# Kernel optimization log

Hardware: AMD Instinct MI355X
Metric: run time of the kernel (lower is better)

The kernel has to match this reference:

```python
import jax, jax.numpy as jnp
import numpy as np

B, S, H = 4, 2048, 1024

def setup_inputs() -> dict:
    key = jax.random.key(0)
    ks = jax.random.split(key, 6)
    scale = 1.0 / np.sqrt(H)
    return {
        "query": jax.random.normal(ks[0], (B, S, H), dtype=jnp.float32),
        "key":   jax.random.normal(ks[1], (B, S, H), dtype=jnp.float32),
        "value": jax.random.normal(ks[2], (B, S, H), dtype=jnp.float32),
        "Wq": jax.random.normal(ks[3], (H, H), dtype=jnp.float32) * scale,
        "Wk": jax.random.normal(ks[4], (H, H), dtype=jnp.float32) * scale,
        "Wv": jax.random.normal(ks[5], (H, H), dtype=jnp.float32) * scale,
    }

def reference(query, key, value, Wq, Wk, Wv):
    # nn.Linear(bias=False): y = x @ W.T
    q = jnp.einsum('bsh,oh->bso', query, Wq)
    k = jnp.einsum('bsh,oh->bso', key, Wk)
    v = jnp.einsum('bsh,oh->bso', value, Wv)
    # full QK^T scores [B, Q, K], scaled by sqrt(hidden_size)
    scores = jnp.einsum('bqh,bkh->bqk', q, k) / jnp.sqrt(jnp.asarray(H, q.dtype))
    attn = jax.nn.softmax(scores, axis=2)
    return jnp.einsum('bqk,bkh->bqh', attn, v)
```

## Files before the change

### kernel.cpp

```cpp
#include <hip/hip_runtime.h>
#include <hip/hip_bf16.h>
#include <stdint.h>

#define BATCH 4
#define SLEN  2048
#define HID   1024

typedef __attribute__((ext_vector_type(8))) short bfrag8;
typedef __attribute__((ext_vector_type(4))) float facc4;
typedef __attribute__((ext_vector_type(4))) unsigned short us4;

__device__ __forceinline__ float b2f(unsigned short u) {
  union { unsigned int i; float f; } x; x.i = ((unsigned int)u) << 16; return x.f;
}
__device__ __forceinline__ unsigned short f2b(float f) {
  union { float f; unsigned int i; } x; x.f = f;
  unsigned int r = x.i + 0x7FFFu + ((x.i >> 16) & 1u);
  return (unsigned short)(r >> 16);
}

__device__ __forceinline__ void gl_lds16(const void* g, void* l) {
  __builtin_amdgcn_global_load_lds(
      (const __attribute__((address_space(1))) void*)g,
      (__attribute__((address_space(3))) void*)l, 16, 0, 0);
}

__global__ __launch_bounds__(256) void cast_all(
    const float* __restrict__ q, const float* __restrict__ k,
    const float* __restrict__ v, const float* __restrict__ wq,
    const float* __restrict__ wk, const float* __restrict__ wv,
    us4* __restrict__ dst) {
  const long i = (long)blockIdx.x * 256 + threadIdx.x;
  const long S1 = 2097152, S2 = 4194304, S3 = 6291456,
             S4 = 6553600, S5 = 6815744;
  const float4* src; long off;
  if (i < S2) {
    if (i < S1) { src = (const float4*)q;  off = i; }
    else        { src = (const float4*)k;  off = i - S1; }
  } else if (i < S3) { src = (const float4*)v;  off = i - S2; }
  else if   (i < S4) { src = (const float4*)wq; off = i - S3; }
  else if   (i < S5) { src = (const float4*)wk; off = i - S4; }
  else               { src = (const float4*)wv; off = i - S5; }
  float4 x = src[off];
  us4 o;
  o.x = f2b(x.x); o.y = f2b(x.y); o.z = f2b(x.z); o.w = f2b(x.w);
  dst[i] = o;
}

__device__ __forceinline__ void store_out(float* p, float v) { *p = v; }
__device__ __forceinline__ void store_out(unsigned short* p, float v) { *p = f2b(v); }

template <typename OutT>
__global__ __launch_bounds__(256) void gemm_nt(
    const unsigned short* __restrict__ A, const unsigned short* __restrict__ B,
    OutT* __restrict__ C, int K, int lda, int ldb, int ldc,
    long aStrideZ, long bStrideZ, long cStrideZ, float alpha) {
  A += (long)blockIdx.z * aStrideZ;
  B += (long)blockIdx.z * bStrideZ;
  C += (long)blockIdx.z * cStrideZ;

  const int nbm = gridDim.x, nbn = gridDim.y;
  const int nb  = nbm * nbn;
  const int pid = blockIdx.y * nbm + blockIdx.x;
  const int p2  = (pid & 7) * (nb >> 3) + (pid >> 3);
  const int GROUP = 4;
  const int gsize = GROUP * nbn;
  const int gid   = p2 / gsize;
  const int rem   = p2 - gid * gsize;
  const long bm = (long)(gid * GROUP + (rem & (GROUP - 1))) * 128;
  const long bn = (long)(rem >> 2) * 128;

  __shared__ __align__(16) unsigned short As[128 * 64];
  __shared__ __align__(16) unsigned short Bs[128 * 64];

  const int tid  = threadIdx.x;
  const int lane = tid & 63;
  const int wave = tid >> 6;
  const int wr   = (wave >> 1) * 64;
  const int wc   = (wave & 1) * 64;
  const int ln   = lane & 15;
  const int lq   = lane >> 4;
  const int swz  = ln & 7;

  facc4 acc[4][4] = {};

  const unsigned short* ap[4]; const unsigned short* bp[4];
  unsigned short* asd[4]; unsigned short* bsd[4];
#pragma unroll
  for (int j = 0; j < 4; ++j) {
    const int c   = j * 256 + tid;
    const int row = c >> 3;
    const int src = ((c & 7) ^ (row & 7)) * 8;
    ap[j]  = A + (bm + row) * (long)lda + src;
    bp[j]  = B + (bn + row) * (long)ldb + src;
    asd[j] = &As[c * 8];
    bsd[j] = &Bs[c * 8];
  }

  for (int k0 = 0; k0 < K; k0 += 64) {
#pragma unroll
    for (int j = 0; j < 4; ++j) { gl_lds16(ap[j], asd[j]); ap[j] += 64; }
#pragma unroll
    for (int j = 0; j < 4; ++j) { gl_lds16(bp[j], bsd[j]); bp[j] += 64; }
    __syncthreads();

#pragma unroll
    for (int kk = 0; kk < 2; ++kk) {
      bfrag8 af[4], bfr[4];
#pragma unroll
      for (int i = 0; i < 4; ++i)
        af[i] = *(const bfrag8*)&As[(wr + i * 16 + ln) * 64 + ((kk * 4 + lq) ^ swz) * 8];
#pragma unroll
      for (int j = 0; j < 4; ++j)
        bfr[j] = *(const bfrag8*)&Bs[(wc + j * 16 + ln) * 64 + ((kk * 4 + lq) ^ swz) * 8];
#pragma unroll
      for (int i = 0; i < 4; ++i)
#pragma unroll
        for (int j = 0; j < 4; ++j)
          acc[i][j] = __builtin_amdgcn_mfma_f32_16x16x32_bf16(af[i], bfr[j], acc[i][j], 0, 0, 0);
    }
    __syncthreads();
  }

#pragma unroll
  for (int i = 0; i < 4; ++i) {
#pragma unroll
    for (int j = 0; j < 4; ++j) {
      const long m = bm + wr + i * 16 + lq * 4;
      const long n = bn + wc + j * 16 + ln;
#pragma unroll
      for (int r = 0; r < 4; ++r)
        store_out(&C[(m + r) * (long)ldc + n], acc[i][j][r] * alpha);
    }
  }
}

__global__ __launch_bounds__(256) void softmax_rows(unsigned short* __restrict__ P) {
  unsigned short* row = P + (long)blockIdx.x * 2048;
  const int t = threadIdx.x;
  const int lane = t & 63, wv = t >> 6;

  bfrag8 v = *(const bfrag8*)(row + t * 8);
  float f[8];
#pragma unroll
  for (int i = 0; i < 8; ++i) f[i] = b2f(((const unsigned short*)&v)[i]);

  float m = f[0];
#pragma unroll
  for (int i = 1; i < 8; ++i) m = fmaxf(m, f[i]);
#pragma unroll
  for (int w = 32; w >= 1; w >>= 1) m = fmaxf(m, __shfl_xor(m, w, 64));
  __shared__ float redm[4];
  if (lane == 0) redm[wv] = m;
  __syncthreads();
  m = fmaxf(fmaxf(redm[0], redm[1]), fmaxf(redm[2], redm[3]));

  float e[8], s = 0.f;
#pragma unroll
  for (int i = 0; i < 8; ++i) { e[i] = __expf(f[i] - m); s += e[i]; }
#pragma unroll
  for (int w = 32; w >= 1; w >>= 1) s += __shfl_xor(s, w, 64);
  __shared__ float reds[4];
  if (lane == 0) reds[wv] = s;
  __syncthreads();
  s = reds[0] + reds[1] + reds[2] + reds[3];
  const float inv = 1.0f / s;

  bfrag8 o;
#pragma unroll
  for (int i = 0; i < 8; ++i) ((unsigned short*)&o)[i] = f2b(e[i] * inv);
  *(bfrag8*)(row + t * 8) = o;
}

extern "C" void kernel_launch(void* const* d_in, const int* in_sizes, int n_in,
                              void* d_out, int out_size, void* d_ws, size_t ws_size,
                              hipStream_t stream) {
  const float* q_in = (const float*)d_in[0];
  const float* k_in = (const float*)d_in[1];
  const float* v_in = (const float*)d_in[2];
  const float* wq   = (const float*)d_in[3];
  const float* wk   = (const float*)d_in[4];
  const float* wv   = (const float*)d_in[5];
  float* out = (float*)d_out;

  const long NXH = (long)BATCH * SLEN * HID;
  const long NW  = (long)HID * HID;
  const long SH  = (long)SLEN * HID;
  const long SS  = (long)SLEN * SLEN;

  unsigned short* ws = (unsigned short*)d_ws;
  unsigned short* Xq  = ws;
  unsigned short* Xk  = Xq  + NXH;
  unsigned short* Xv  = Xk  + NXH;
  unsigned short* Wqb = Xv  + NXH;
  unsigned short* Wkb = Wqb + NW;
  unsigned short* Wvb = Wkb + NW;
  unsigned short* Qb  = Wvb + NW;
  unsigned short* Kb  = Qb  + NXH;
  unsigned short* Vt  = Kb  + NXH;
  unsigned short* P   = Xq;

  const dim3 blk(256);

  cast_all<<<dim3(27648), blk, 0, stream>>>(q_in, k_in, v_in, wq, wk, wv, (us4*)ws);

  gemm_nt<unsigned short><<<dim3(64, 8, 2), blk, 0, stream>>>(
      Xq, Wqb, Qb, HID, HID, HID, HID, NXH, NW, NXH, 1.0f);
  gemm_nt<unsigned short><<<dim3(8, 64, 1), blk, 0, stream>>>(
      Wvb, Xv, Vt, HID, HID, HID, BATCH * SLEN, 0, 0, 0, 1.0f);

  gemm_nt<unsigned short><<<dim3(16, 16, BATCH), blk, 0, stream>>>(
      Qb, Kb, P, HID, HID, HID, SLEN, SH, SH, SS, 0.03125f);

  softmax_rows<<<dim3(BATCH * SLEN), blk, 0, stream>>>(P);

  gemm_nt<float><<<dim3(16, 8, BATCH), blk, 0, stream>>>(
      P, Vt, out, SLEN, SLEN, BATCH * SLEN, HID, SS, SLEN, SH, 1.0f);
}
```

Before: 319.8 us.

## Double-buffer GEMM LDS tiles with K=32 steps and manual waitcnt pipelining

Splits the shared-memory A/B tiles into two K=32 buffers and prefetches the next tile with direct global-to-LDS loads while MFMAs run on the current one. Partial vmcnt waits plus raw barriers replace the full __syncthreads so loads overlap compute. The LDS swizzle is rewritten for the 32-wide rows to avoid bank conflicts. In exchange there are twice as many loop iterations and barriers, each with less work, and the correctness of the hand-encoded waitcnt values depends on in-order completion of the global loads.

```diff
diff --git a/kernel.cpp b/kernel.cpp
--- a/kernel.cpp
+++ b/kernel.cpp
@@ -9,6 +9,10 @@
 typedef __attribute__((ext_vector_type(8))) short bfrag8;
 typedef __attribute__((ext_vector_type(4))) float facc4;
 typedef __attribute__((ext_vector_type(4))) unsigned short us4;
+
+#define WAIT_VM4   0x0F74
+#define WAIT_VM0   0x0F70
+#define WAIT_LGKM0 0xC07F
 
 __device__ __forceinline__ float b2f(unsigned short u) {
   union { unsigned int i; float f; } x; x.i = ((unsigned int)u) << 16; return x.f;
@@ -70,8 +74,8 @@
   const long bm = (long)(gid * GROUP + (rem & (GROUP - 1))) * 128;
   const long bn = (long)(rem >> 2) * 128;
 
-  __shared__ __align__(16) unsigned short As[128 * 64];
-  __shared__ __align__(16) unsigned short Bs[128 * 64];
+  __shared__ __align__(16) unsigned short As[2][128 * 32];
+  __shared__ __align__(16) unsigned short Bs[2][128 * 32];
 
   const int tid  = threadIdx.x;
   const int lane = tid & 63;
@@ -80,46 +84,56 @@
   const int wc   = (wave & 1) * 64;
   const int ln   = lane & 15;
   const int lq   = lane >> 4;
-  const int swz  = ln & 7;
+  const int cs   = (lq ^ ((ln ^ (ln >> 2)) & 3)) * 8;
 
   facc4 acc[4][4] = {};
 
-  const unsigned short* ap[4]; const unsigned short* bp[4];
-  unsigned short* asd[4]; unsigned short* bsd[4];
-#pragma unroll
-  for (int j = 0; j < 4; ++j) {
-    const int c   = j * 256 + tid;
-    const int row = c >> 3;
-    const int src = ((c & 7) ^ (row & 7)) * 8;
-    ap[j]  = A + (bm + row) * (long)lda + src;
-    bp[j]  = B + (bn + row) * (long)ldb + src;
-    asd[j] = &As[c * 8];
-    bsd[j] = &Bs[c * 8];
-  }
-
-  for (int k0 = 0; k0 < K; k0 += 64) {
-#pragma unroll
-    for (int j = 0; j < 4; ++j) { gl_lds16(ap[j], asd[j]); ap[j] += 64; }
-#pragma unroll
-    for (int j = 0; j < 4; ++j) { gl_lds16(bp[j], bsd[j]); bp[j] += 64; }
-    __syncthreads();
-
-#pragma unroll
-    for (int kk = 0; kk < 2; ++kk) {
-      bfrag8 af[4], bfr[4];
-#pragma unroll
-      for (int i = 0; i < 4; ++i)
-        af[i] = *(const bfrag8*)&As[(wr + i * 16 + ln) * 64 + ((kk * 4 + lq) ^ swz) * 8];
-#pragma unroll
-      for (int j = 0; j < 4; ++j)
-        bfr[j] = *(const bfrag8*)&Bs[(wc + j * 16 + ln) * 64 + ((kk * 4 + lq) ^ swz) * 8];
-#pragma unroll
-      for (int i = 0; i < 4; ++i)
-#pragma unroll
-        for (int j = 0; j < 4; ++j)
-          acc[i][j] = __builtin_amdgcn_mfma_f32_16x16x32_bf16(af[i], bfr[j], acc[i][j], 0, 0, 0);
+  const int s0 = tid, s1 = 256 + tid;
+  const int r0 = s0 >> 2, r1 = s1 >> 2;
+  const int p0 = (((s0 & 3) ^ ((r0 ^ (r0 >> 2)) & 3))) * 8;
+  const int p1 = (((s1 & 3) ^ ((r1 ^ (r1 >> 2)) & 3))) * 8;
+  const unsigned short* a0 = A + (bm + r0) * (long)lda + p0;
+  const unsigned short* a1 = A + (bm + r1) * (long)lda + p1;
+  const unsigned short* b0 = B + (bn + r0) * (long)ldb + p0;
+  const unsigned short* b1 = B + (bn + r1) * (long)ldb + p1;
+
+  const int NIT = K >> 5;
+
+  gl_lds16(a0, &As[0][s0 * 8]);
+  gl_lds16(a1, &As[0][s1 * 8]);
+  gl_lds16(b0, &Bs[0][s0 * 8]);
+  gl_lds16(b1, &Bs[0][s1 * 8]);
+  a0 += 32; a1 += 32; b0 += 32; b1 += 32;
+
+  for (int i = 0; i < NIT; ++i) {
+    const int cur = i & 1, nxt = cur ^ 1;
+    if (i + 1 < NIT) {
+      gl_lds16(a0, &As[nxt][s0 * 8]);
+      gl_lds16(a1, &As[nxt][s1 * 8]);
+      gl_lds16(b0, &Bs[nxt][s0 * 8]);
+      gl_lds16(b1, &Bs[nxt][s1 * 8]);
+      a0 += 32; a1 += 32; b0 += 32; b1 += 32;
+      __builtin_amdgcn_s_waitcnt(WAIT_VM4);
+    } else {
+      __builtin_amdgcn_s_waitcnt(WAIT_VM0);
     }
-    __syncthreads();
+    __builtin_amdgcn_s_barrier();
+
+    bfrag8 af[4], bfr[4];
+#pragma unroll
+    for (int ii = 0; ii < 4; ++ii)
+      af[ii] = *(const bfrag8*)&As[cur][(wr + ii * 16 + ln) * 32 + cs];
+#pragma unroll
+    for (int jj = 0; jj < 4; ++jj)
+      bfr[jj] = *(const bfrag8*)&Bs[cur][(wc + jj * 16 + ln) * 32 + cs];
+#pragma unroll
+    for (int ii = 0; ii < 4; ++ii)
+#pragma unroll
+      for (int jj = 0; jj < 4; ++jj)
+        acc[ii][jj] = __builtin_amdgcn_mfma_f32_16x16x32_bf16(af[ii], bfr[jj], acc[ii][jj], 0, 0, 0);
+
+    __builtin_amdgcn_s_waitcnt(WAIT_LGKM0);
+    __builtin_amdgcn_s_barrier();
   }
 
 #pragma unroll
```

Measured after the change: 334.6 us. +4.6%, slower.
